# Kernel tuning notes

Hardware: AMD Instinct MI355X
Metric: run time of the kernel (lower is better)

Reference implementation:

```python
import jax, jax.numpy as jnp
import numpy as np

D_MODEL = 1024
NUM_HEADS = 16
D_K = D_MODEL // NUM_HEADS


def setup_inputs() -> dict:
    key = jax.random.key(0)
    ks = jax.random.split(key, 9)
    B, S = 2, 2048
    s_in = 1.0 / np.sqrt(D_MODEL)
    x = jax.random.normal(ks[0], (B, S, D_MODEL), dtype=jnp.float32)
    # Linear weights stored as (in_features, out_features): y = x @ W + b
    Wq = jax.random.uniform(ks[1], (D_MODEL, D_MODEL), jnp.float32, -s_in, s_in)
    bq = jax.random.uniform(ks[2], (D_MODEL,), jnp.float32, -s_in, s_in)
    Wk = jax.random.uniform(ks[3], (D_MODEL, D_K), jnp.float32, -s_in, s_in)
    bk = jax.random.uniform(ks[4], (D_K,), jnp.float32, -s_in, s_in)
    Wv = jax.random.uniform(ks[5], (D_MODEL, D_K), jnp.float32, -s_in, s_in)
    bv = jax.random.uniform(ks[6], (D_K,), jnp.float32, -s_in, s_in)
    Wo = jax.random.uniform(ks[7], (D_MODEL, D_MODEL), jnp.float32, -s_in, s_in)
    bo = jax.random.uniform(ks[8], (D_MODEL,), jnp.float32, -s_in, s_in)
    return {"x": x, "Wq": Wq, "bq": bq, "Wk": Wk, "bk": bk,
            "Wv": Wv, "bv": bv, "Wo": Wo, "bo": bo}


def reference(x, Wq, bq, Wk, bk, Wv, bv, Wo, bo):
    B, S, _ = x.shape
    H, Dk = NUM_HEADS, D_K
    # Projections
    Q = (x @ Wq + bq).reshape(B, S, H, Dk).transpose(0, 2, 1, 3)  # [B,H,S,Dk]
    K = x @ Wk + bk                                               # [B,S,Dk] single KV head
    V = x @ Wv + bv                                               # [B,S,Dk]
    # Scores: query heads broadcast against the single shared KV head
    scores = jnp.einsum('bhqd,bkd->bhqk', Q, K) / jnp.sqrt(jnp.float32(Dk))
    attn = jax.nn.softmax(scores, axis=-1)                        # [B,H,S,S]
    out = jnp.einsum('bhqk,bkd->bhqd', attn, V)                   # [B,H,S,Dk]
    out = out.transpose(0, 2, 1, 3).reshape(B, S, H * Dk)         # [B,S,d_model]
    return out @ Wo + bo
```

## Files before the change

### kernel.cpp

```cpp
#include <hip/hip_runtime.h>
#include <hip/hip_bf16.h>

typedef __attribute__((ext_vector_type(8))) short bf16x8;
typedef __attribute__((ext_vector_type(4))) float f32x4;
typedef __attribute__((ext_vector_type(16))) float f32x16;
typedef __attribute__((ext_vector_type(4))) unsigned short ushort4v;

#define QSCALE 0.1803368801111204f

__device__ __forceinline__ unsigned short f2bf(float f) {
  union { float f; unsigned int u; } x; x.f = f;
  unsigned int u = x.u;
  unsigned int r = (u + 0x7fffu + ((u >> 16) & 1u)) >> 16;
  return (unsigned short)r;
}

__device__ __forceinline__ unsigned short cvt1bf(float a) {
  union { __hip_bfloat162 h; unsigned short s[2]; } c;
  c.h = __float22bfloat162_rn(make_float2(a, a));
  return c.s[0];
}

__global__ __launch_bounds__(256) void prep_kernel(
    const float* __restrict__ x,
    const float* __restrict__ Wq, const float* __restrict__ Wk,
    const float* __restrict__ Wv, const float* __restrict__ Wo,
    unsigned short* __restrict__ xb,
    unsigned short* __restrict__ QKVt, unsigned short* __restrict__ Wot) {
  int z = blockIdx.z;
  if (z == 4) {
    size_t base = ((size_t)(blockIdx.y * 32 + blockIdx.x)) * 4096 + threadIdx.x * 16;
#pragma unroll
    for (int c = 0; c < 4; ++c) {
      float4 v = *(const float4*)(x + base + c * 4);
      ushort4v o = { f2bf(v.x), f2bf(v.y), f2bf(v.z), f2bf(v.w) };
      *(ushort4v*)(xb + base + c * 4) = o;
    }
    return;
  }
  __shared__ float t[32][33];
  const float* src;
  unsigned short* dst;
  int C, rowoff;
  if (z == 0)      { src = Wq; dst = QKVt; C = 1024; rowoff = 0; }
  else if (z == 1) { src = Wk; dst = QKVt; C = 64;   rowoff = 1024; }
  else if (z == 2) { src = Wv; dst = QKVt; C = 64;   rowoff = 1088; }
  else             { src = Wo; dst = Wot;  C = 1024; rowoff = 0; }
  int c0 = blockIdx.x * 32, r0 = blockIdx.y * 32;
  if (c0 >= C) return;
  int tx = threadIdx.x & 31, ty = threadIdx.x >> 5;
#pragma unroll
  for (int i = 0; i < 32; i += 8)
    t[ty + i][tx] = src[(size_t)(r0 + ty + i) * C + c0 + tx];
  __syncthreads();
#pragma unroll
  for (int i = 0; i < 32; i += 8)
    dst[(size_t)(rowoff + c0 + ty + i) * 1024 + r0 + tx] = f2bf(t[tx][ty + i]);
}

template <typename OutT, bool QKVMODE>
__global__ __launch_bounds__(256) void gemm_bf16_kernel(
    const unsigned short* __restrict__ A, const unsigned short* __restrict__ Bt,
    const float* __restrict__ b0, const float* __restrict__ b1,
    const float* __restrict__ b2, OutT* __restrict__ C,
    unsigned short* __restrict__ Vt, int M, int N, int K) {
  constexpr int LS = 40;
  __shared__ unsigned short As[2][128 * LS];
  __shared__ unsigned short Bs[2][64 * LS];
  int tid = threadIdx.x;
  int wid = tid >> 6, lane = tid & 63;
  int l15 = lane & 15, quad = lane >> 4;
  int m0 = blockIdx.x * 128, n0 = blockIdx.y * 64;
  int mw = (wid >> 1) * 64, nw = (wid & 1) * 32;
  f32x4 acc[4][2];
#pragma unroll
  for (int i = 0; i < 4; i++)
#pragma unroll
    for (int j = 0; j < 2; j++)
#pragma unroll
      for (int e = 0; e < 4; ++e) acc[i][j][e] = 0.f;

  int arow = tid >> 2, akc = (tid & 3) * 8;
  const unsigned short* Ag = A + (size_t)(m0 + arow) * K + akc;
  const unsigned short* Bg = Bt + (size_t)(n0 + arow) * K + akc;
  bf16x8 ar0 = *(const bf16x8*)(Ag);
  bf16x8 ar1 = *(const bf16x8*)(Ag + (size_t)64 * K);
  bf16x8 br0 = *(const bf16x8*)(Bg);

  for (int k0 = 0; k0 < K; k0 += 32) {
    unsigned short* Asb = As[(k0 >> 5) & 1];
    unsigned short* Bsb = Bs[(k0 >> 5) & 1];
    *(bf16x8*)(Asb + arow * LS + akc) = ar0;
    *(bf16x8*)(Asb + (arow + 64) * LS + akc) = ar1;
    *(bf16x8*)(Bsb + arow * LS + akc) = br0;
    __syncthreads();
    if (k0 + 32 < K) {
      ar0 = *(const bf16x8*)(Ag + k0 + 32);
      ar1 = *(const bf16x8*)(Ag + (size_t)64 * K + k0 + 32);
      br0 = *(const bf16x8*)(Bg + k0 + 32);
    }
    bf16x8 af[4], bfr[2];
#pragma unroll
    for (int t = 0; t < 4; ++t)
      af[t] = *(const bf16x8*)(Asb + (mw + t * 16 + l15) * LS + quad * 8);
#pragma unroll
    for (int t = 0; t < 2; ++t)
      bfr[t] = *(const bf16x8*)(Bsb + (nw + t * 16 + l15) * LS + quad * 8);
#pragma unroll
    for (int mt = 0; mt < 4; ++mt)
#pragma unroll
      for (int nt = 0; nt < 2; ++nt)
        acc[mt][nt] = __builtin_amdgcn_mfma_f32_16x16x32_bf16(
            af[mt], bfr[nt], acc[mt][nt], 0, 0, 0);
  }
#pragma unroll
  for (int mt = 0; mt < 4; ++mt)
#pragma unroll
    for (int nt = 0; nt < 2; ++nt) {
      int col = n0 + nw + nt * 16 + l15;
      float bias, cs;
      if constexpr (QKVMODE) {
        bias = (col < 1024) ? b0[col] : ((col < 1088) ? b1[col - 1024] : b2[col - 1088]);
        cs = (col < 1024) ? QSCALE : 1.0f;
      } else {
        bias = b0[col];
        cs = 1.0f;
      }
#pragma unroll
      for (int r = 0; r < 4; ++r) {
        int row = m0 + mw + mt * 16 + quad * 4 + r;
        float v = (acc[mt][nt][r] + bias) * cs;
        if constexpr (sizeof(OutT) == 2)
          C[(size_t)row * N + col] = f2bf(v);
        else
          C[(size_t)row * N + col] = v;
        if constexpr (QKVMODE) {
          if (col >= 1088)
            Vt[((size_t)(row >> 11) * 64 + (col - 1088)) * 2048 + (row & 2047)] =
                f2bf(v);
        }
      }
    }
}

__global__ __launch_bounds__(512, 4) void flash_attn_kernel(
    const unsigned short* __restrict__ QKV,
    const unsigned short* __restrict__ Vt,
    unsigned short* __restrict__ AO) {
  constexpr int S = 2048, LDQ = 1152;
  constexpr int PK = 72, PP = 72;
  __shared__ unsigned short Ks[2][64 * PK];
  __shared__ unsigned short Vs[2][64 * PK];
  __shared__ unsigned short Ps[8][32 * PP];
  int tid = threadIdx.x;
  int wid = tid >> 6, lane = tid & 63;
  int l31 = lane & 31, half = lane >> 5;
  int p = wid & 3, ks = wid >> 2;
  int q0 = blockIdx.x * 128, h = blockIdx.y, b = blockIdx.z;

  const unsigned short* Qb =
      QKV + (size_t)(b * S + q0 + p * 32 + l31) * LDQ + h * 64 + half * 8;
  bf16x8 qf[4];
#pragma unroll
  for (int f = 0; f < 4; ++f) qf[f] = *(const bf16x8*)(Qb + f * 16);

  int u = tid & 255, sl = tid >> 8;
  int srow = u >> 2, sc = (u & 3) * 8;
  const unsigned short* Kgb = QKV + ((size_t)b * S) * LDQ + 1024;
  const unsigned short* Vgb = Vt + ((size_t)(b * 64 + srow)) * 2048;

  f32x16 oa0, oa1;
#pragma unroll
  for (int r = 0; r < 16; ++r) { oa0[r] = 0.f; oa1[r] = 0.f; }
  float rs[16];
#pragma unroll
  for (int r = 0; r < 16; ++r) rs[r] = 0.f;

  int kb0 = sl * 1024;
  bf16x8 ka = *(const bf16x8*)(Kgb + (size_t)(kb0 + srow) * LDQ + sc);
  bf16x8 kc = *(const bf16x8*)(Kgb + (size_t)(kb0 + srow) * LDQ + sc + 32);
  bf16x8 va = *(const bf16x8*)(Vgb + kb0 + sc);
  bf16x8 vc = *(const bf16x8*)(Vgb + kb0 + sc + 32);

  unsigned short* Pw = Ps[wid];
  unsigned short* Ksb = Ks[ks];
  unsigned short* Vsb = Vs[ks];

  for (int kt = 0; kt < 16; ++kt) {
    *(bf16x8*)(Ks[sl] + srow * PK + sc) = ka;
    *(bf16x8*)(Ks[sl] + srow * PK + sc + 32) = kc;
    *(bf16x8*)(Vs[sl] + srow * PK + sc) = va;
    *(bf16x8*)(Vs[sl] + srow * PK + sc + 32) = vc;
    __syncthreads();
    if (kt + 1 < 16) {
      int kbn = sl * 1024 + (kt + 1) * 64;
      ka = *(const bf16x8*)(Kgb + (size_t)(kbn + srow) * LDQ + sc);
      kc = *(const bf16x8*)(Kgb + (size_t)(kbn + srow) * LDQ + sc + 32);
      va = *(const bf16x8*)(Vgb + kbn + sc);
      vc = *(const bf16x8*)(Vgb + kbn + sc + 32);
    }

#pragma unroll
    for (int n2 = 0; n2 < 2; ++n2) {
      f32x16 sacc;
#pragma unroll
      for (int i = 0; i < 16; ++i) sacc[i] = 0.f;
#pragma unroll
      for (int s = 0; s < 4; ++s) {
        bf16x8 kf =
            *(const bf16x8*)(Ksb + (n2 * 32 + l31) * PK + s * 16 + half * 8);
        sacc = __builtin_amdgcn_mfma_f32_32x32x16_bf16(qf[s], kf, sacc, 0, 0, 0);
      }
#pragma unroll
      for (int r = 0; r < 16; ++r) {
        float pr = __builtin_amdgcn_exp2f(sacc[r]);
        rs[r] += pr;
        int row = (r & 3) + 8 * (r >> 2) + 4 * half;
        Pw[row * PP + n2 * 32 + l31] = cvt1bf(pr);
      }
    }

    bf16x8 pf[4];
#pragma unroll
    for (int s = 0; s < 4; ++s)
      pf[s] = *(const bf16x8*)(Pw + l31 * PP + s * 16 + half * 8);
#pragma unroll
    for (int s = 0; s < 4; ++s) {
      bf16x8 vf0 = *(const bf16x8*)(Vsb + (l31)*PK + s * 16 + half * 8);
      bf16x8 vf1 = *(const bf16x8*)(Vsb + (32 + l31) * PK + s * 16 + half * 8);
      oa0 = __builtin_amdgcn_mfma_f32_32x32x16_bf16(pf[s], vf0, oa0, 0, 0, 0);
      oa1 = __builtin_amdgcn_mfma_f32_32x32x16_bf16(pf[s], vf1, oa1, 0, 0, 0);
    }
    __syncthreads();
  }

#pragma unroll
  for (int r = 0; r < 16; ++r) {
    float t = rs[r];
    t += __shfl_xor(t, 1, 32);
    t += __shfl_xor(t, 2, 32);
    t += __shfl_xor(t, 4, 32);
    t += __shfl_xor(t, 8, 32);
    t += __shfl_xor(t, 16, 32);
    rs[r] = t;
  }

  float* Cb = (float*)Ps;
  if (ks == 1) {
#pragma unroll
    for (int r = 0; r < 16; ++r) {
      int row = (r & 3) + 8 * (r >> 2) + 4 * half;
      Cb[(p * 32 + row) * 65 + l31] = oa0[r];
      Cb[(p * 32 + row) * 65 + 32 + l31] = oa1[r];
      if (l31 == 0) Cb[(p * 32 + row) * 65 + 64] = rs[r];
    }
  }
  __syncthreads();
  if (ks == 0) {
    unsigned short* Ob = AO + (size_t)(b * S + q0 + p * 32) * 1024 + h * 64;
#pragma unroll
    for (int r = 0; r < 16; ++r) {
      int row = (r & 3) + 8 * (r >> 2) + 4 * half;
      float p0 = Cb[(p * 32 + row) * 65 + l31];
      float p1 = Cb[(p * 32 + row) * 65 + 32 + l31];
      float rsu = Cb[(p * 32 + row) * 65 + 64];
      float inv = 1.0f / (rs[r] + rsu);
      Ob[(size_t)row * 1024 + l31] = f2bf((oa0[r] + p0) * inv);
      Ob[(size_t)row * 1024 + 32 + l31] = f2bf((oa1[r] + p1) * inv);
    }
  }
}

extern "C" void kernel_launch(void* const* d_in, const int* in_sizes, int n_in,
                              void* d_out, int out_size, void* d_ws, size_t ws_size,
                              hipStream_t stream) {
  const float* x  = (const float*)d_in[0];
  const float* Wq = (const float*)d_in[1];
  const float* bq = (const float*)d_in[2];
  const float* Wk = (const float*)d_in[3];
  const float* bk = (const float*)d_in[4];
  const float* Wv = (const float*)d_in[5];
  const float* bv = (const float*)d_in[6];
  const float* Wo = (const float*)d_in[7];
  const float* bo = (const float*)d_in[8];
  float* out = (float*)d_out;

  constexpr int B = 2, S = 2048, D = 1024, Dk = 64, H = 16;
  constexpr int M = B * S;
  constexpr int NQKV = D + 2 * Dk;

  char* ws = (char*)d_ws;
  unsigned short* xb   = (unsigned short*)ws; ws += (size_t)M * D * 2;
  unsigned short* QKVt = (unsigned short*)ws; ws += (size_t)NQKV * D * 2;
  unsigned short* Wot  = (unsigned short*)ws; ws += (size_t)D * D * 2;
  unsigned short* QKV  = (unsigned short*)ws; ws += (size_t)M * NQKV * 2;
  unsigned short* Vtb  = (unsigned short*)ws; ws += (size_t)B * Dk * S * 2;
  unsigned short* AO   = (unsigned short*)ws; ws += (size_t)M * D * 2;

  prep_kernel<<<dim3(32, 32, 5), 256, 0, stream>>>(x, Wq, Wk, Wv, Wo, xb, QKVt, Wot);

  gemm_bf16_kernel<unsigned short, true><<<dim3(M / 128, NQKV / 64), 256, 0, stream>>>(
      xb, QKVt, bq, bk, bv, QKV, Vtb, M, NQKV, D);

  flash_attn_kernel<<<dim3(S / 128, H, B), 512, 0, stream>>>(QKV, Vtb, AO);

  gemm_bf16_kernel<float, false><<<dim3(M / 128, D / 64), 256, 0, stream>>>(
      AO, Wot, bo, nullptr, nullptr, out, nullptr, M, D, D);
}
```

Measured before the change: 187.7 us.

## Load GEMM tiles via direct global-to-LDS loads and widen output GEMM tile

Replaces the register-staged, double-buffered LDS tile loads in the bf16 GEMM with global_load_lds direct transfers into an unpadded single LDS buffer, adding a second barrier per k-step. The GEMM is templated on BN, and the output projection now uses 128x128 tiles. This is meant to cut register traffic and VGPR pressure and to improve reuse in the output GEMM. In exchange it loses load/compute overlap and the LDS padding, so bank conflicts become possible.

Measured after the change: 191.9 us. +2.2%, slower.

```diff
diff --git a/kernel.cpp b/kernel.cpp
--- a/kernel.cpp
+++ b/kernel.cpp
@@ -19,6 +19,12 @@
   union { __hip_bfloat162 h; unsigned short s[2]; } c;
   c.h = __float22bfloat162_rn(make_float2(a, a));
   return c.s[0];
+}
+
+__device__ __forceinline__ void gll16(const unsigned short* g, unsigned short* l) {
+  __builtin_amdgcn_global_load_lds(
+      (const __attribute__((address_space(1))) unsigned int*)g,
+      (__attribute__((address_space(3))) unsigned int*)l, 16, 0, 0);
 }
 
 __global__ __launch_bounds__(256) void prep_kernel(
@@ -58,65 +64,58 @@
     dst[(size_t)(rowoff + c0 + ty + i) * 1024 + r0 + tx] = f2bf(t[tx][ty + i]);
 }
 
-template <typename OutT, bool QKVMODE>
+template <int BN, typename OutT, bool QKVMODE>
 __global__ __launch_bounds__(256) void gemm_bf16_kernel(
     const unsigned short* __restrict__ A, const unsigned short* __restrict__ Bt,
     const float* __restrict__ b0, const float* __restrict__ b1,
     const float* __restrict__ b2, OutT* __restrict__ C,
     unsigned short* __restrict__ Vt, int M, int N, int K) {
-  constexpr int LS = 40;
-  __shared__ unsigned short As[2][128 * LS];
-  __shared__ unsigned short Bs[2][64 * LS];
+  constexpr int NT = BN / 32;
+  __shared__ __align__(16) unsigned short As[128 * 32];
+  __shared__ __align__(16) unsigned short Bs[BN * 32];
   int tid = threadIdx.x;
   int wid = tid >> 6, lane = tid & 63;
   int l15 = lane & 15, quad = lane >> 4;
-  int m0 = blockIdx.x * 128, n0 = blockIdx.y * 64;
-  int mw = (wid >> 1) * 64, nw = (wid & 1) * 32;
-  f32x4 acc[4][2];
+  int m0 = blockIdx.x * 128, n0 = blockIdx.y * BN;
+  int mw = (wid >> 1) * 64, nw = (wid & 1) * (BN / 2);
+  f32x4 acc[4][NT];
 #pragma unroll
   for (int i = 0; i < 4; i++)
 #pragma unroll
-    for (int j = 0; j < 2; j++)
+    for (int j = 0; j < NT; j++)
 #pragma unroll
       for (int e = 0; e < 4; ++e) acc[i][j][e] = 0.f;
 
-  int arow = tid >> 2, akc = (tid & 3) * 8;
-  const unsigned short* Ag = A + (size_t)(m0 + arow) * K + akc;
-  const unsigned short* Bg = Bt + (size_t)(n0 + arow) * K + akc;
-  bf16x8 ar0 = *(const bf16x8*)(Ag);
-  bf16x8 ar1 = *(const bf16x8*)(Ag + (size_t)64 * K);
-  bf16x8 br0 = *(const bf16x8*)(Bg);
+  const unsigned short* Ag = A + (size_t)(m0 + (tid >> 2)) * K + (tid & 3) * 8;
+  const unsigned short* Bg = Bt + (size_t)(n0 + (tid >> 2)) * K + (tid & 3) * 8;
+  unsigned short* Asd = As + tid * 8;
+  unsigned short* Bsd = Bs + tid * 8;
 
   for (int k0 = 0; k0 < K; k0 += 32) {
-    unsigned short* Asb = As[(k0 >> 5) & 1];
-    unsigned short* Bsb = Bs[(k0 >> 5) & 1];
-    *(bf16x8*)(Asb + arow * LS + akc) = ar0;
-    *(bf16x8*)(Asb + (arow + 64) * LS + akc) = ar1;
-    *(bf16x8*)(Bsb + arow * LS + akc) = br0;
+    gll16(Ag + k0, Asd);
+    gll16(Ag + (size_t)64 * K + k0, Asd + 256 * 8);
+    gll16(Bg + k0, Bsd);
+    if constexpr (BN == 128) gll16(Bg + (size_t)64 * K + k0, Bsd + 256 * 8);
     __syncthreads();
-    if (k0 + 32 < K) {
-      ar0 = *(const bf16x8*)(Ag + k0 + 32);
-      ar1 = *(const bf16x8*)(Ag + (size_t)64 * K + k0 + 32);
-      br0 = *(const bf16x8*)(Bg + k0 + 32);
-    }
-    bf16x8 af[4], bfr[2];
+    bf16x8 af[4], bfr[NT];
 #pragma unroll
     for (int t = 0; t < 4; ++t)
-      af[t] = *(const bf16x8*)(Asb + (mw + t * 16 + l15) * LS + quad * 8);
-#pragma unroll
-    for (int t = 0; t < 2; ++t)
-      bfr[t] = *(const bf16x8*)(Bsb + (nw + t * 16 + l15) * LS + quad * 8);
+      af[t] = *(const bf16x8*)(As + (mw + t * 16 + l15) * 32 + quad * 8);
+#pragma unroll
+    for (int t = 0; t < NT; ++t)
+      bfr[t] = *(const bf16x8*)(Bs + (nw + t * 16 + l15) * 32 + quad * 8);
 #pragma unroll
     for (int mt = 0; mt < 4; ++mt)
 #pragma unroll
-      for (int nt = 0; nt < 2; ++nt)
+      for (int nt = 0; nt < NT; ++nt)
         acc[mt][nt] = __builtin_amdgcn_mfma_f32_16x16x32_bf16(
             af[mt], bfr[nt], acc[mt][nt], 0, 0, 0);
+    __syncthreads();
   }
 #pragma unroll
   for (int mt = 0; mt < 4; ++mt)
 #pragma unroll
-    for (int nt = 0; nt < 2; ++nt) {
+    for (int nt = 0; nt < NT; ++nt) {
       int col = n0 + nw + nt * 16 + l15;
       float bias, cs;
       if constexpr (QKVMODE) {
@@ -299,11 +298,11 @@
 
   prep_kernel<<<dim3(32, 32, 5), 256, 0, stream>>>(x, Wq, Wk, Wv, Wo, xb, QKVt, Wot);
 
-  gemm_bf16_kernel<unsigned short, true><<<dim3(M / 128, NQKV / 64), 256, 0, stream>>>(
+  gemm_bf16_kernel<64, unsigned short, true><<<dim3(M / 128, NQKV / 64), 256, 0, stream>>>(
       xb, QKVt, bq, bk, bv, QKV, Vtb, M, NQKV, D);
 
   flash_attn_kernel<<<dim3(S / 128, H, B), 512, 0, stream>>>(QKV, Vtb, AO);
 
-  gemm_bf16_kernel<float, false><<<dim3(M / 128, D / 64), 256, 0, stream>>>(
+  gemm_bf16_kernel<128, float, false><<<dim3(M / 128, D / 128), 256, 0, stream>>>(
       AO, Wot, bo, nullptr, nullptr, out, nullptr, M, D, D);
 }
```

## Load GEMM tiles directly into LDS with global_load_lds double buffering

Applied to the files above, without the earlier changes.

Replaces the register-staged global-to-LDS copies in the bf16 GEMM with direct global_load_lds transfers into a double-buffered unpadded LDS tile, using manual vmcnt waits and two barriers per k-step. This removes the VGPR round trip and the separate LDS store instructions. In exchange the padding is dropped, so the LDS fragment reads may hit more bank conflicts, and an extra barrier is added each iteration.

After: 185.9 us. No clear change (-0.9%).

```diff
diff --git a/kernel.cpp b/kernel.cpp
--- a/kernel.cpp
+++ b/kernel.cpp
@@ -19,6 +19,12 @@
   union { __hip_bfloat162 h; unsigned short s[2]; } c;
   c.h = __float22bfloat162_rn(make_float2(a, a));
   return c.s[0];
+}
+
+__device__ __forceinline__ void gll16(const unsigned short* g, unsigned short* l) {
+  __builtin_amdgcn_global_load_lds(
+      (const __attribute__((address_space(1))) unsigned int*)g,
+      (__attribute__((address_space(3))) unsigned int*)l, 16, 0, 0);
 }
 
 __global__ __launch_bounds__(256) void prep_kernel(
@@ -64,9 +70,8 @@
     const float* __restrict__ b0, const float* __restrict__ b1,
     const float* __restrict__ b2, OutT* __restrict__ C,
     unsigned short* __restrict__ Vt, int M, int N, int K) {
-  constexpr int LS = 40;
-  __shared__ unsigned short As[2][128 * LS];
-  __shared__ unsigned short Bs[2][64 * LS];
+  __shared__ __align__(16) unsigned short As[2][128 * 32];
+  __shared__ __align__(16) unsigned short Bs[2][64 * 32];
   int tid = threadIdx.x;
   int wid = tid >> 6, lane = tid & 63;
   int l15 = lane & 15, quad = lane >> 4;
@@ -80,38 +85,44 @@
 #pragma unroll
       for (int e = 0; e < 4; ++e) acc[i][j][e] = 0.f;
 
-  int arow = tid >> 2, akc = (tid & 3) * 8;
-  const unsigned short* Ag = A + (size_t)(m0 + arow) * K + akc;
-  const unsigned short* Bg = Bt + (size_t)(n0 + arow) * K + akc;
-  bf16x8 ar0 = *(const bf16x8*)(Ag);
-  bf16x8 ar1 = *(const bf16x8*)(Ag + (size_t)64 * K);
-  bf16x8 br0 = *(const bf16x8*)(Bg);
+  const unsigned short* Ag = A + (size_t)(m0 + (tid >> 2)) * K + (tid & 3) * 8;
+  const unsigned short* Bg = Bt + (size_t)(n0 + (tid >> 2)) * K + (tid & 3) * 8;
+
+  gll16(Ag, As[0] + tid * 8);
+  gll16(Ag + (size_t)64 * K, As[0] + 2048 + tid * 8);
+  gll16(Bg, Bs[0] + tid * 8);
 
   for (int k0 = 0; k0 < K; k0 += 32) {
-    unsigned short* Asb = As[(k0 >> 5) & 1];
-    unsigned short* Bsb = Bs[(k0 >> 5) & 1];
-    *(bf16x8*)(Asb + arow * LS + akc) = ar0;
-    *(bf16x8*)(Asb + (arow + 64) * LS + akc) = ar1;
-    *(bf16x8*)(Bsb + arow * LS + akc) = br0;
-    __syncthreads();
+    int cur = (k0 >> 5) & 1;
     if (k0 + 32 < K) {
-      ar0 = *(const bf16x8*)(Ag + k0 + 32);
-      ar1 = *(const bf16x8*)(Ag + (size_t)64 * K + k0 + 32);
-      br0 = *(const bf16x8*)(Bg + k0 + 32);
-    }
+      int nxt = cur ^ 1;
+      gll16(Ag + k0 + 32, As[nxt] + tid * 8);
+      gll16(Ag + (size_t)64 * K + k0 + 32, As[nxt] + 2048 + tid * 8);
+      gll16(Bg + k0 + 32, Bs[nxt] + tid * 8);
+      asm volatile("s_waitcnt vmcnt(3)" ::: "memory");
+    } else {
+      asm volatile("s_waitcnt vmcnt(0)" ::: "memory");
+    }
+    __builtin_amdgcn_s_barrier();
+    __builtin_amdgcn_sched_barrier(0);
+    const unsigned short* Asb = As[cur];
+    const unsigned short* Bsb = Bs[cur];
     bf16x8 af[4], bfr[2];
 #pragma unroll
     for (int t = 0; t < 4; ++t)
-      af[t] = *(const bf16x8*)(Asb + (mw + t * 16 + l15) * LS + quad * 8);
+      af[t] = *(const bf16x8*)(Asb + (mw + t * 16 + l15) * 32 + quad * 8);
 #pragma unroll
     for (int t = 0; t < 2; ++t)
-      bfr[t] = *(const bf16x8*)(Bsb + (nw + t * 16 + l15) * LS + quad * 8);
+      bfr[t] = *(const bf16x8*)(Bsb + (nw + t * 16 + l15) * 32 + quad * 8);
 #pragma unroll
     for (int mt = 0; mt < 4; ++mt)
 #pragma unroll
       for (int nt = 0; nt < 2; ++nt)
         acc[mt][nt] = __builtin_amdgcn_mfma_f32_16x16x32_bf16(
             af[mt], bfr[nt], acc[mt][nt], 0, 0, 0);
+    asm volatile("s_waitcnt lgkmcnt(0)" ::: "memory");
+    __builtin_amdgcn_sched_barrier(0);
+    __builtin_amdgcn_s_barrier();
   }
 #pragma unroll
   for (int mt = 0; mt < 4; ++mt)
```
